# Performance work log

Measured on AMD Instinct MI355X. Metric: run time of the kernel, lower is better.

Reference implementation:

```python
import jax, jax.numpy as jnp
import numpy as np

NUM_HEADS = 16


def setup_inputs() -> dict:
    key = jax.random.key(0)
    k1, k2, k3 = jax.random.split(key, 3)
    b, s, d_model = 4, 4096, 1024
    x = jax.random.normal(k1, (b, s, d_model), dtype=jnp.float32)
    w_qkv = jax.random.normal(k2, (3 * d_model, d_model), dtype=jnp.float32) * 0.02
    b_qkv = jnp.zeros((3 * d_model,), dtype=jnp.float32)
    w_out = jax.random.normal(k3, (d_model, d_model), dtype=jnp.float32) * 0.02
    b_out = jnp.zeros((d_model,), dtype=jnp.float32)
    return {"x": x, "w_qkv": w_qkv, "b_qkv": b_qkv, "w_out": w_out, "b_out": b_out}


def reference(x, w_qkv, b_qkv, w_out, b_out):
    b, s, d_model = x.shape
    h = NUM_HEADS
    hd = d_model // h
    # qkv projection: [b, s, 3*d_model]
    qkv = jnp.einsum('bsd,ed->bse', x, w_qkv) + b_qkv
    # rearrange 'b s (three h d) -> three b h s d'
    qkv = qkv.reshape(b, s, 3, h, hd).transpose(2, 0, 3, 1, 4)  # [3, b, h, s, hd]
    q, k, v = qkv[0], qkv[1], qkv[2]
    # elu feature map
    q = jax.nn.elu(q) + 1.0
    k = jax.nn.elu(k) + 1.0
    # kv state: [b, h, hd, hd]
    kv = jnp.einsum('bhsd,bhse->bhde', k, v)
    # output: [b, h, s, hd]
    out = jnp.einsum('bhsd,bhde->bhse', q, kv)
    # normalization (elementwise divide by per-feature k sum, broadcast over s)
    k_sum = k.sum(axis=-2, keepdims=True)  # [b, h, 1, hd]
    out = out / (k_sum + 1e-6)
    # 'b h s d -> b s (h d)'
    out = out.transpose(0, 2, 1, 3).reshape(b, s, d_model)
    return jnp.einsum('bsd,ed->bse', out, w_out) + b_out
```

## Files before the change

### kernel.cpp

```cpp
#include <hip/hip_runtime.h>
#include <stdint.h>

typedef float f32x4 __attribute__((ext_vector_type(4)));
typedef __bf16 bf16x8 __attribute__((ext_vector_type(8)));
typedef unsigned short u16;
typedef u16 u16x8 __attribute__((ext_vector_type(8)));

__device__ __forceinline__ u16 f2bf(float f) {
  uint32_t u = __builtin_bit_cast(uint32_t, f);
  return (u16)((u + 0x7fffu + ((u >> 16) & 1u)) >> 16);
}
__device__ __forceinline__ float bf2f(u16 h) {
  uint32_t u = ((uint32_t)h) << 16;
  return __builtin_bit_cast(float, u);
}
__device__ __forceinline__ float elup1(float x) {
  return x > 0.f ? x + 1.f : __expf(x);
}
__device__ __forceinline__ void gll16(const void* g, void* l) {
  __builtin_amdgcn_global_load_lds(
      (const __attribute__((address_space(1))) unsigned int*)g,
      (__attribute__((address_space(3))) unsigned int*)l, 16, 0, 0);
}

#define BAR() __builtin_amdgcn_s_barrier()
#define VMC(n) asm volatile("s_waitcnt vmcnt(" #n ")" ::: "memory")

__global__ void cvt_all_kernel(const float* __restrict__ x, u16* __restrict__ xb,
                               const float* __restrict__ wq, u16* __restrict__ wqb,
                               const float* __restrict__ wo, u16* __restrict__ wob) {
  int i = blockIdx.x * 256 + threadIdx.x;
  const float* in;
  u16* out;
  if (i < 4194304) {
    in = x; out = xb;
  } else if (i < 4980736) {
    in = wq; out = wqb; i -= 4194304;
  } else {
    in = wo; out = wob; i -= 4980736;
  }
  float4 f = ((const float4*)in)[i];
  ushort4 o;
  o.x = f2bf(f.x); o.y = f2bf(f.y); o.z = f2bf(f.z); o.w = f2bf(f.w);
  ((ushort4*)out)[i] = o;
}

template <int EPI>
__global__ __launch_bounds__(512, 2)
void gemm256(const u16* __restrict__ A, const u16* __restrict__ B,
             const float* __restrict__ bias, void* __restrict__ Cout,
             int N, int K, int nbj) {
  __shared__ __align__(16) u16 lds[65536];
  const int tid = threadIdx.x;
  const int wave = tid >> 6, lane = tid & 63;
  const int fr = lane & 15, fq = lane >> 4;
  const int wm = wave >> 2, wn = wave & 3;

  const int nwg = gridDim.x;
  const int cpx = nwg >> 3;
  const int swz = (blockIdx.x & 7) * cpx + (blockIdx.x >> 3);
  const int bi = swz / nbj, bj = swz % nbj;

  const u16* Ab = A + (size_t)bi * 256 * K;
  const u16* Bb = B + (size_t)bj * 256 * K;

  const int l8 = lane >> 3;
  const int cswz = ((lane & 7) ^ l8) << 3;
  const int r6 = wave * 8 + l8;

#define STAGE_A(d, h, k0)                                                      \
  { _Pragma("unroll")                                                          \
    for (int i_ = 0; i_ < 2; ++i_) {                                           \
      int gr_ = i_ * 128 + (h) * 64 + r6;                                      \
      gll16(Ab + (size_t)gr_ * K + (k0) + cswz,                                \
            &lds[((d) * 32768 + (h) * 16384 + i_ * 8192 + wave * 1024) >> 1]); \
    } }

#define STAGE_B(d, h, k0)                                                      \
  { _Pragma("unroll")                                                          \
    for (int i_ = 0; i_ < 2; ++i_) {                                           \
      int r_ = i_ * 64 + r6;                                                   \
      int gr_ = (r_ >> 5) * 64 + (h) * 32 + (r_ & 31);                         \
      gll16(Bb + (size_t)gr_ * K + (k0) + cswz,                                \
            &lds[(65536 + (d) * 32768 + (h) * 16384 + i_ * 8192 + wave * 1024) >> 1]); \
    } }

  const int xorc = (fr & 7) << 4;
  const int acol[2] = {(fq * 16) ^ xorc, (64 + fq * 16) ^ xorc};
  const int arow = (wm * 64 + fr) * 128;
  const int brow = (wn * 32 + fr) * 128;

#define LDSV(off) (*(const bf16x8*)&lds[(off) >> 1])

  f32x4 acc[8][4] = {};
  bf16x8 af[4][2];
  bf16x8 bfr[2][2][2];

#define READ_A(d, mh)                                                          \
  { _Pragma("unroll")                                                          \
    for (int ks = 0; ks < 2; ++ks) {                                           \
      _Pragma("unroll")                                                        \
      for (int mm = 0; mm < 4; ++mm)                                           \
        af[mm][ks] = LDSV((d) * 32768 + (mh) * 16384 + arow + mm * 2048 + acol[ks]); \
    } }

#define READ_B(d, nh)                                                          \
  { _Pragma("unroll")                                                          \
    for (int ks = 0; ks < 2; ++ks) {                                           \
      _Pragma("unroll")                                                        \
      for (int nn = 0; nn < 2; ++nn)                                           \
        bfr[nh][nn][ks] = LDSV(65536 + (d) * 32768 + (nh) * 16384 + brow + nn * 2048 + acol[ks]); \
    } }

#define MFMA_Q(mh, nh)                                                         \
  { __builtin_amdgcn_s_setprio(1);                                             \
    _Pragma("unroll")                                                          \
    for (int ks = 0; ks < 2; ++ks) {                                           \
      _Pragma("unroll")                                                        \
      for (int mm = 0; mm < 4; ++mm) {                                         \
        _Pragma("unroll")                                                      \
        for (int nn = 0; nn < 2; ++nn)                                         \
          acc[(mh) * 4 + mm][(nh) * 2 + nn] = __builtin_amdgcn_mfma_f32_16x16x32_bf16( \
              af[mm][ks], bfr[nh][nn][ks], acc[(mh) * 4 + mm][(nh) * 2 + nn], 0, 0, 0); \
      } }                                                                      \
    __builtin_amdgcn_s_setprio(0); }

  const int NT = K >> 6;
  STAGE_A(0, 0, 0); STAGE_B(0, 0, 0); STAGE_B(0, 1, 0); STAGE_A(0, 1, 0);
  STAGE_A(1, 0, 64); STAGE_B(1, 0, 64); STAGE_B(1, 1, 64);
  VMC(6);
  BAR();

  for (int t = 0; t < NT; ++t) {
    const int d = t & 1;
    const int k1 = (t + 1) << 6, k2 = (t + 2) << 6;
    if (t + 1 < NT) STAGE_A(d ^ 1, 1, k1);
    READ_B(d, 0); READ_A(d, 0);
    MFMA_Q(0, 0);
    READ_B(d, 1);
    MFMA_Q(0, 1);
    BAR();
    if (t + 2 < NT) { STAGE_A(d, 0, k2); STAGE_B(d, 0, k2); }
    READ_A(d, 1);
    MFMA_Q(1, 1);
    if (t + 2 < NT) STAGE_B(d, 1, k2);
    MFMA_Q(1, 0);
    if (t < NT - 2) { VMC(6); } else { VMC(0); }
    BAR();
  }

  const int wrow = wm * 128, wcol = wn * 64;
  if (EPI == 0) {
    const bool do_elu = (bj * 256) < 2048;
    float bv[4];
#pragma unroll
    for (int n = 0; n < 4; ++n) bv[n] = bias[bj * 256 + wcol + n * 16 + fr];
    u16* wbuf = &lds[wave * 8192];
    const int lrow = lane >> 3, lcol = (lane & 7) * 8;
#pragma unroll
    for (int ch = 0; ch < 2; ++ch) {
#pragma unroll
      for (int m2 = 0; m2 < 4; ++m2)
#pragma unroll
        for (int n = 0; n < 4; ++n)
#pragma unroll
          for (int r = 0; r < 4; ++r) {
            float v = acc[ch * 4 + m2][n][r] + bv[n];
            if (do_elu) v = elup1(v);
            wbuf[(m2 * 16 + fq * 4 + r) * 72 + n * 16 + fr] = f2bf(v);
          }
#pragma unroll
      for (int i = 0; i < 8; ++i) {
        bf16x8 val = *(const bf16x8*)&wbuf[(i * 8 + lrow) * 72 + lcol];
        const int rowg = bi * 256 + wrow + ch * 64 + i * 8 + lrow;
        *(bf16x8*)&((u16*)Cout)[(size_t)rowg * N + bj * 256 + wcol + lcol] = val;
      }
    }
  } else {
#pragma unroll
    for (int n = 0; n < 4; ++n) {
      const int colg = bj * 256 + wcol + n * 16 + fr;
      const float bv = bias[colg];
#pragma unroll
      for (int m = 0; m < 8; ++m)
#pragma unroll
        for (int r = 0; r < 4; ++r) {
          const int rowg = bi * 256 + wrow + m * 16 + fq * 4 + r;
          ((float*)Cout)[(size_t)rowg * N + colg] = acc[m][n][r] + bv;
        }
    }
  }
#undef STAGE_A
#undef STAGE_B
#undef READ_A
#undef READ_B
#undef MFMA_Q
#undef LDSV
}

__global__ __launch_bounds__(256)
void kv_state_kernel(const u16* __restrict__ qkv, float* __restrict__ pkv,
                     float* __restrict__ pks) {
  const int bh = blockIdx.x, chunk = blockIdx.y;
  const int b = bh >> 4, h = bh & 15;
  const int t = threadIdx.x;
  __shared__ float sK[16][68];
  __shared__ float sV[16][68];
  const int dg = (t & 15) * 4;
  const int eg = (t >> 4) * 4;
  f32x4 acc0 = {}, acc1 = {}, acc2 = {}, acc3 = {};
  f32x4 ak4 = {};
  const size_t rowbase = ((size_t)b * 4096 + (size_t)chunk * 512) * 3072;
  const u16* kp = qkv + rowbase + 1024 + h * 64;
  const u16* vp = qkv + rowbase + 2048 + h * 64;
  const int lhalf = t >> 7, lr = (t >> 3) & 15, lc = (t & 7) * 8;
  const u16* lsrc = lhalf ? vp : kp;
  float* ldst = lhalf ? &sV[lr][lc] : &sK[lr][lc];
  for (int s0 = 0; s0 < 512; s0 += 16) {
    u16x8 v8 = *(const u16x8*)&lsrc[(size_t)(s0 + lr) * 3072 + lc];
#pragma unroll
    for (int j = 0; j < 8; ++j) ldst[j] = bf2f(v8[j]);
    __syncthreads();
#pragma unroll 4
    for (int sl = 0; sl < 16; ++sl) {
      const f32x4 kv4 = *(const f32x4*)&sK[sl][dg];
      const f32x4 vv4 = *(const f32x4*)&sV[sl][eg];
      acc0 += kv4[0] * vv4;
      acc1 += kv4[1] * vv4;
      acc2 += kv4[2] * vv4;
      acc3 += kv4[3] * vv4;
      ak4 += kv4;
    }
    __syncthreads();
  }
  float* outp = pkv + ((size_t)chunk * 64 + bh) * 4096;
  *(f32x4*)&outp[(dg + 0) * 64 + eg] = acc0;
  *(f32x4*)&outp[(dg + 1) * 64 + eg] = acc1;
  *(f32x4*)&outp[(dg + 2) * 64 + eg] = acc2;
  *(f32x4*)&outp[(dg + 3) * 64 + eg] = acc3;
  if (t < 16) *(f32x4*)&pks[((size_t)chunk * 64 + bh) * 64 + dg] = ak4;
}

__global__ __launch_bounds__(256)
void kv_reduce_kernel(const float* __restrict__ pkv, const float* __restrict__ pks,
                      float* __restrict__ kvn) {
  const int bh = blockIdx.x;
  const int t = threadIdx.x;
  __shared__ float sks[64];
  if (t < 64) {
    float s = 0.f;
    for (int c = 0; c < 8; ++c) s += pks[((size_t)c * 64 + bh) * 64 + t];
    sks[t] = s + 1e-6f;
  }
  __syncthreads();
#pragma unroll
  for (int j = 0; j < 16; ++j) {
    int idx = t + j * 256;
    float s = 0.f;
    for (int c = 0; c < 8; ++c) s += pkv[((size_t)c * 64 + bh) * 4096 + idx];
    kvn[(size_t)bh * 4096 + idx] = s / sks[idx & 63];
  }
}

__global__ __launch_bounds__(256)
void attn_out_kernel(const u16* __restrict__ qkv, const float* __restrict__ kvn,
                     u16* __restrict__ attn) {
  const int bh = blockIdx.x;
  const int b = bh >> 4, h = bh & 15;
  const int stile = blockIdx.y;
  const int wave = threadIdx.x >> 6, lane = threadIdx.x & 63;
  const int s0 = stile * 64 + wave * 16;
  const int fr = lane & 15, fq = lane >> 4;
  __shared__ u16 sO[4][16 * 72];
  const float* kv = kvn + (size_t)bh * 4096;
  bf16x8 bfrag[2][4];
#pragma unroll
  for (int ks = 0; ks < 2; ++ks)
#pragma unroll
    for (int n = 0; n < 4; ++n) {
      u16x8 tmp;
#pragma unroll
      for (int j = 0; j < 8; ++j)
        tmp[j] = f2bf(kv[(size_t)(ks * 32 + fq * 8 + j) * 64 + n * 16 + fr]);
      bfrag[ks][n] = __builtin_bit_cast(bf16x8, tmp);
    }
  const u16* q = qkv + (size_t)b * 4096 * 3072 + h * 64;
  f32x4 acc[4] = {};
#pragma unroll
  for (int ks = 0; ks < 2; ++ks) {
    bf16x8 af = *(const bf16x8*)&q[(size_t)(s0 + fr) * 3072 + ks * 32 + fq * 8];
#pragma unroll
    for (int n = 0; n < 4; ++n)
      acc[n] = __builtin_amdgcn_mfma_f32_16x16x32_bf16(af, bfrag[ks][n], acc[n], 0, 0, 0);
  }
  u16* wb = &sO[wave][0];
#pragma unroll
  for (int n = 0; n < 4; ++n)
#pragma unroll
    for (int r = 0; r < 4; ++r)
      wb[(fq * 4 + r) * 72 + n * 16 + fr] = f2bf(acc[n][r]);
  u16* ap = attn + (size_t)b * 4096 * 1024 + h * 64;
  const int lrow = lane >> 3, lcol = (lane & 7) * 8;
#pragma unroll
  for (int i = 0; i < 2; ++i) {
    bf16x8 val = *(const bf16x8*)&wb[(i * 8 + lrow) * 72 + lcol];
    *(bf16x8*)&ap[(size_t)(s0 + i * 8 + lrow) * 1024 + lcol] = val;
  }
}

extern "C" void kernel_launch(void* const* d_in, const int* in_sizes, int n_in,
                              void* d_out, int out_size, void* d_ws, size_t ws_size,
                              hipStream_t stream) {
  const float* x     = (const float*)d_in[0];
  const float* w_qkv = (const float*)d_in[1];
  const float* b_qkv = (const float*)d_in[2];
  const float* w_out = (const float*)d_in[3];
  const float* b_out = (const float*)d_in[4];
  float* out = (float*)d_out;

  const int M = 16384, Dm = 1024, N3 = 3072;

  char* ws = (char*)d_ws;
  u16* xb     = (u16*)(ws);
  u16* wqb    = (u16*)(ws + 33554432);
  u16* wob    = (u16*)(ws + 39845888);
  u16* qkvb   = (u16*)(ws + 41943040);
  u16* attnb  = (u16*)(ws + 142606336);
  float* pkv  = (float*)(ws + 176160768);
  float* pks  = (float*)(ws + 184549376);
  float* kvn  = (float*)(ws + 184680448);

  cvt_all_kernel<<<20480, 256, 0, stream>>>(x, xb, w_qkv, wqb, w_out, wob);

  gemm256<0><<<(M / 256) * (N3 / 256), 512, 0, stream>>>(xb, wqb, b_qkv, qkvb, N3, Dm, N3 / 256);
  kv_state_kernel<<<dim3(64, 8), 256, 0, stream>>>(qkvb, pkv, pks);
  kv_reduce_kernel<<<64, 256, 0, stream>>>(pkv, pks, kvn);
  attn_out_kernel<<<dim3(64, 64), 256, 0, stream>>>(qkvb, kvn, attnb);
  gemm256<1><<<(M / 256) * (Dm / 256), 512, 0, stream>>>(attnb, wob, b_out, out, Dm, Dm, Dm / 256);
}
```

Before: 241.7 us.

## Fold KV state into per-batch output weights and restructure GEMM pipeline

Instead of computing attn = Q·KVn and then attn·W_out^T, the output weights are pre-multiplied per batch by the normalized KV state (W2 = W_out·KVn^T per head), so the final GEMM reads Q directly from the qkv buffer with a stride of 3072 and a per-batch B matrix. This removes the attn_out kernel and its intermediate write/read. The GEMM main loop is also rewritten as a single-buffer-ahead schedule with waves alternating which A half they compute first, and it waits for all loads each iteration. That schedule change may reduce overlap compared with the previous two-stage prefetch.

```diff
diff --git a/kernel.cpp b/kernel.cpp
--- a/kernel.cpp
+++ b/kernel.cpp
@@ -47,9 +47,9 @@
 
 template <int EPI>
 __global__ __launch_bounds__(512, 2)
-void gemm256(const u16* __restrict__ A, const u16* __restrict__ B,
+void gemm256(const u16* __restrict__ A, int lda, const u16* __restrict__ B,
              const float* __restrict__ bias, void* __restrict__ Cout,
-             int N, int K, int nbj) {
+             int N, int K, int nbj, int bstep) {
   __shared__ __align__(16) u16 lds[65536];
   const int tid = threadIdx.x;
   const int wave = tid >> 6, lane = tid & 63;
@@ -61,8 +61,8 @@
   const int swz = (blockIdx.x & 7) * cpx + (blockIdx.x >> 3);
   const int bi = swz / nbj, bj = swz % nbj;
 
-  const u16* Ab = A + (size_t)bi * 256 * K;
-  const u16* Bb = B + (size_t)bj * 256 * K;
+  const u16* Ab = A + (size_t)bi * 256 * lda;
+  const u16* Bb = B + (size_t)(bi >> 4) * bstep + (size_t)bj * 256 * K;
 
   const int l8 = lane >> 3;
   const int cswz = ((lane & 7) ^ l8) << 3;
@@ -72,7 +72,7 @@
   { _Pragma("unroll")                                                          \
     for (int i_ = 0; i_ < 2; ++i_) {                                           \
       int gr_ = i_ * 128 + (h) * 64 + r6;                                      \
-      gll16(Ab + (size_t)gr_ * K + (k0) + cswz,                                \
+      gll16(Ab + (size_t)gr_ * lda + (k0) + cswz,                              \
             &lds[((d) * 32768 + (h) * 16384 + i_ * 8192 + wave * 1024) >> 1]); \
     } }
 
@@ -85,6 +85,9 @@
             &lds[(65536 + (d) * 32768 + (h) * 16384 + i_ * 8192 + wave * 1024) >> 1]); \
     } }
 
+#define STAGE_ALL(d, k0) \
+  { STAGE_A(d, 0, k0); STAGE_A(d, 1, k0); STAGE_B(d, 0, k0); STAGE_B(d, 1, k0); }
+
   const int xorc = (fr & 7) << 4;
   const int acol[2] = {(fq * 16) ^ xorc, (64 + fq * 16) ^ xorc};
   const int arow = (wm * 64 + fr) * 128;
@@ -93,15 +96,15 @@
 #define LDSV(off) (*(const bf16x8*)&lds[(off) >> 1])
 
   f32x4 acc[8][4] = {};
-  bf16x8 af[4][2];
+  bf16x8 af0[4][2], af1[4][2];
   bf16x8 bfr[2][2][2];
 
-#define READ_A(d, mh)                                                          \
+#define READ_A(d, mh, dst)                                                     \
   { _Pragma("unroll")                                                          \
     for (int ks = 0; ks < 2; ++ks) {                                           \
       _Pragma("unroll")                                                        \
       for (int mm = 0; mm < 4; ++mm)                                           \
-        af[mm][ks] = LDSV((d) * 32768 + (mh) * 16384 + arow + mm * 2048 + acol[ks]); \
+        dst[mm][ks] = LDSV((d) * 32768 + (mh) * 16384 + arow + mm * 2048 + acol[ks]); \
     } }
 
 #define READ_B(d, nh)                                                          \
@@ -112,7 +115,7 @@
         bfr[nh][nn][ks] = LDSV(65536 + (d) * 32768 + (nh) * 16384 + brow + nn * 2048 + acol[ks]); \
     } }
 
-#define MFMA_Q(mh, nh)                                                         \
+#define MFMA_Q(mh, nh, src)                                                    \
   { __builtin_amdgcn_s_setprio(1);                                             \
     _Pragma("unroll")                                                          \
     for (int ks = 0; ks < 2; ++ks) {                                           \
@@ -121,32 +124,38 @@
         _Pragma("unroll")                                                      \
         for (int nn = 0; nn < 2; ++nn)                                         \
           acc[(mh) * 4 + mm][(nh) * 2 + nn] = __builtin_amdgcn_mfma_f32_16x16x32_bf16( \
-              af[mm][ks], bfr[nh][nn][ks], acc[(mh) * 4 + mm][(nh) * 2 + nn], 0, 0, 0); \
+              src[mm][ks], bfr[nh][nn][ks], acc[(mh) * 4 + mm][(nh) * 2 + nn], 0, 0, 0); \
       } }                                                                      \
     __builtin_amdgcn_s_setprio(0); }
 
+#define TILE_BODY(F, S, afF, afS, d, t)                                        \
+  {                                                                            \
+    READ_B(d, 0); READ_B(d, 1); READ_A(d, F, afF);                             \
+    MFMA_Q(F, 0, afF);                                                         \
+    READ_A(d, S, afS);                                                         \
+    MFMA_Q(F, 1, afF);                                                         \
+    if ((t) + 1 < NT) STAGE_ALL((d) ^ 1, ((t) + 1) << 6);                      \
+    MFMA_Q(S, 1, afS);                                                         \
+    MFMA_Q(S, 0, afS);                                                         \
+  }
+
   const int NT = K >> 6;
-  STAGE_A(0, 0, 0); STAGE_B(0, 0, 0); STAGE_B(0, 1, 0); STAGE_A(0, 1, 0);
-  STAGE_A(1, 0, 64); STAGE_B(1, 0, 64); STAGE_B(1, 1, 64);
-  VMC(6);
+  STAGE_ALL(0, 0);
+  VMC(0);
   BAR();
 
-  for (int t = 0; t < NT; ++t) {
-    const int d = t & 1;
-    const int k1 = (t + 1) << 6, k2 = (t + 2) << 6;
-    if (t + 1 < NT) STAGE_A(d ^ 1, 1, k1);
-    READ_B(d, 0); READ_A(d, 0);
-    MFMA_Q(0, 0);
-    READ_B(d, 1);
-    MFMA_Q(0, 1);
-    BAR();
-    if (t + 2 < NT) { STAGE_A(d, 0, k2); STAGE_B(d, 0, k2); }
-    READ_A(d, 1);
-    MFMA_Q(1, 1);
-    if (t + 2 < NT) STAGE_B(d, 1, k2);
-    MFMA_Q(1, 0);
-    if (t < NT - 2) { VMC(6); } else { VMC(0); }
-    BAR();
+  if ((wave & 1) == 0) {
+    for (int t = 0; t < NT; ++t) {
+      const int d = t & 1;
+      TILE_BODY(0, 1, af0, af1, d, t);
+      VMC(0); BAR();
+    }
+  } else {
+    for (int t = 0; t < NT; ++t) {
+      const int d = t & 1;
+      TILE_BODY(1, 0, af1, af0, d, t);
+      VMC(0); BAR();
+    }
   }
 
   const int wrow = wm * 128, wcol = wn * 64;
@@ -192,9 +201,11 @@
   }
 #undef STAGE_A
 #undef STAGE_B
+#undef STAGE_ALL
 #undef READ_A
 #undef READ_B
 #undef MFMA_Q
+#undef TILE_BODY
 #undef LDSV
 }
 
@@ -243,7 +254,7 @@
 
 __global__ __launch_bounds__(256)
 void kv_reduce_kernel(const float* __restrict__ pkv, const float* __restrict__ pks,
-                      float* __restrict__ kvn) {
+                      u16* __restrict__ kvnb) {
   const int bh = blockIdx.x;
   const int t = threadIdx.x;
   __shared__ float sks[64];
@@ -258,53 +269,51 @@
     int idx = t + j * 256;
     float s = 0.f;
     for (int c = 0; c < 8; ++c) s += pkv[((size_t)c * 64 + bh) * 4096 + idx];
-    kvn[(size_t)bh * 4096 + idx] = s / sks[idx & 63];
+    kvnb[(size_t)bh * 4096 + idx] = f2bf(s / sks[idx & 63]);
   }
 }
 
 __global__ __launch_bounds__(256)
-void attn_out_kernel(const u16* __restrict__ qkv, const float* __restrict__ kvn,
-                     u16* __restrict__ attn) {
+void w2t_kernel(const u16* __restrict__ wob, const u16* __restrict__ kvnb,
+                u16* __restrict__ w2t) {
   const int bh = blockIdx.x;
   const int b = bh >> 4, h = bh & 15;
-  const int stile = blockIdx.y;
   const int wave = threadIdx.x >> 6, lane = threadIdx.x & 63;
-  const int s0 = stile * 64 + wave * 16;
   const int fr = lane & 15, fq = lane >> 4;
-  __shared__ u16 sO[4][16 * 72];
-  const float* kv = kvn + (size_t)bh * 4096;
-  bf16x8 bfrag[2][4];
+  const int j0 = blockIdx.y * 256 + wave * 64;
+  __shared__ u16 sW[4][16 * 72];
+  const u16* kvp = kvnb + (size_t)bh * 4096;
+  bf16x8 bfr[4][2];
 #pragma unroll
   for (int ks = 0; ks < 2; ++ks)
 #pragma unroll
-    for (int n = 0; n < 4; ++n) {
-      u16x8 tmp;
-#pragma unroll
-      for (int j = 0; j < 8; ++j)
-        tmp[j] = f2bf(kv[(size_t)(ks * 32 + fq * 8 + j) * 64 + n * 16 + fr]);
-      bfrag[ks][n] = __builtin_bit_cast(bf16x8, tmp);
-    }
-  const u16* q = qkv + (size_t)b * 4096 * 3072 + h * 64;
-  f32x4 acc[4] = {};
-#pragma unroll
-  for (int ks = 0; ks < 2; ++ks) {
-    bf16x8 af = *(const bf16x8*)&q[(size_t)(s0 + fr) * 3072 + ks * 32 + fq * 8];
-#pragma unroll
-    for (int n = 0; n < 4; ++n)
-      acc[n] = __builtin_amdgcn_mfma_f32_16x16x32_bf16(af, bfrag[ks][n], acc[n], 0, 0, 0);
-  }
-  u16* wb = &sO[wave][0];
-#pragma unroll
-  for (int n = 0; n < 4; ++n)
-#pragma unroll
-    for (int r = 0; r < 4; ++r)
-      wb[(fq * 4 + r) * 72 + n * 16 + fr] = f2bf(acc[n][r]);
-  u16* ap = attn + (size_t)b * 4096 * 1024 + h * 64;
+    for (int nn = 0; nn < 4; ++nn)
+      bfr[nn][ks] = *(const bf16x8*)&kvp[(nn * 16 + fr) * 64 + ks * 32 + fq * 8];
+  f32x4 acc[4][4] = {};
+#pragma unroll
+  for (int mm = 0; mm < 4; ++mm)
+#pragma unroll
+    for (int ks = 0; ks < 2; ++ks) {
+      bf16x8 af = *(const bf16x8*)&wob[(size_t)(j0 + mm * 16 + fr) * 1024 + h * 64 + ks * 32 + fq * 8];
+#pragma unroll
+      for (int nn = 0; nn < 4; ++nn)
+        acc[mm][nn] = __builtin_amdgcn_mfma_f32_16x16x32_bf16(af, bfr[nn][ks], acc[mm][nn], 0, 0, 0);
+    }
+  u16* wb = &sW[wave][0];
+  u16* op = w2t + (size_t)b * 1048576 + h * 64;
   const int lrow = lane >> 3, lcol = (lane & 7) * 8;
 #pragma unroll
-  for (int i = 0; i < 2; ++i) {
-    bf16x8 val = *(const bf16x8*)&wb[(i * 8 + lrow) * 72 + lcol];
-    *(bf16x8*)&ap[(size_t)(s0 + i * 8 + lrow) * 1024 + lcol] = val;
+  for (int mm = 0; mm < 4; ++mm) {
+#pragma unroll
+    for (int nn = 0; nn < 4; ++nn)
+#pragma unroll
+      for (int r = 0; r < 4; ++r)
+        wb[(fq * 4 + r) * 72 + nn * 16 + fr] = f2bf(acc[mm][nn][r]);
+#pragma unroll
+    for (int i = 0; i < 2; ++i) {
+      bf16x8 val = *(const bf16x8*)&wb[(i * 8 + lrow) * 72 + lcol];
+      *(bf16x8*)&op[(size_t)(j0 + mm * 16 + i * 8 + lrow) * 1024 + lcol] = val;
+    }
   }
 }
 
@@ -325,16 +334,18 @@
   u16* wqb    = (u16*)(ws + 33554432);
   u16* wob    = (u16*)(ws + 39845888);
   u16* qkvb   = (u16*)(ws + 41943040);
-  u16* attnb  = (u16*)(ws + 142606336);
+  u16* w2t    = (u16*)(ws + 142606336);
   float* pkv  = (float*)(ws + 176160768);
   float* pks  = (float*)(ws + 184549376);
-  float* kvn  = (float*)(ws + 184680448);
+  u16* kvnb   = (u16*)(ws + 184680448);
 
   cvt_all_kernel<<<20480, 256, 0, stream>>>(x, xb, w_qkv, wqb, w_out, wob);
 
-  gemm256<0><<<(M / 256) * (N3 / 256), 512, 0, stream>>>(xb, wqb, b_qkv, qkvb, N3, Dm, N3 / 256);
+  gemm256<0><<<(M / 256) * (N3 / 256), 512, 0, stream>>>(
+      xb, Dm, wqb, b_qkv, qkvb, N3, Dm, N3 / 256, 0);
   kv_state_kernel<<<dim3(64, 8), 256, 0, stream>>>(qkvb, pkv, pks);
-  kv_reduce_kernel<<<64, 256, 0, stream>>>(pkv, pks, kvn);
-  attn_out_kernel<<<dim3(64, 64), 256, 0, stream>>>(qkvb, kvn, attnb);
-  gemm256<1><<<(M / 256) * (Dm / 256), 512, 0, stream>>>(attnb, wob, b_out, out, Dm, Dm, Dm / 256);
-}
+  kv_reduce_kernel<<<64, 256, 0, stream>>>(pkv, pks, kvnb);
+  w2t_kernel<<<dim3(64, 4), 256, 0, stream>>>(wob, kvnb, w2t);
+  gemm256<1><<<(M / 256) * (Dm / 256), 512, 0, stream>>>(
+      qkvb, N3, w2t, b_out, out, Dm, Dm, Dm / 256, 1 << 20);
+}
```

Measured after the change: 225.0 us. -6.9%, faster.
